# Optimization experiments

Measured on AMD Instinct MI355X. Metric: run time of the kernel, lower is better.

Reference implementation:

```python
import jax, jax.numpy as jnp
import numpy as np

TOTAL_WORDS = 10000
EMBED_LEN = 100
SEQ_LEN = 200
BATCH = 128
UNITS = 256


def setup_inputs() -> dict:
    key = jax.random.key(0)
    ks = jax.random.split(key, 8)
    inputs = jax.random.randint(ks[0], (BATCH, SEQ_LEN), 0, TOTAL_WORDS, dtype=jnp.int32)
    emb = jax.random.normal(ks[1], (TOTAL_WORDS, EMBED_LEN), dtype=jnp.float32) * 0.05
    kernel = jax.random.normal(ks[2], (EMBED_LEN, 3 * UNITS), dtype=jnp.float32) * 0.05
    rkernel = jax.random.normal(ks[3], (UNITS, 3 * UNITS), dtype=jnp.float32) * 0.05
    bias_i = jnp.zeros((3 * UNITS,), dtype=jnp.float32)
    bias_r = jnp.zeros((3 * UNITS,), dtype=jnp.float32)
    w_out = jax.random.normal(ks[4], (UNITS, 1), dtype=jnp.float32) * 0.05
    b_out = jnp.zeros((1,), dtype=jnp.float32)
    return {"inputs": inputs, "emb": emb, "kernel": kernel, "rkernel": rkernel,
            "bias_i": bias_i, "bias_r": bias_r, "w_out": w_out, "b_out": b_out}


def _gru_step(x_t, h, kernel, rkernel, bias_i, bias_r):
    # Keras GRUCell with reset_after=True (TF2 default)
    mx = x_t @ kernel + bias_i          # [B, 3U]
    mh = h @ rkernel + bias_r           # [B, 3U]
    xz, xr, xh = jnp.split(mx, 3, axis=-1)
    hz, hr, hh = jnp.split(mh, 3, axis=-1)
    z = jax.nn.sigmoid(xz + hz)
    r = jax.nn.sigmoid(xr + hr)
    cand = jnp.tanh(xh + r * hh)
    return z * h + (1.0 - z) * cand


def reference(inputs, emb, kernel, rkernel, bias_i, bias_r, w_out, b_out):
    x = emb[inputs]                     # [B, T, E]
    xt = jnp.transpose(x, (1, 0, 2))    # [T, B, E]
    h0 = jnp.zeros((inputs.shape[0], UNITS), dtype=emb.dtype)
    h1 = jnp.zeros((inputs.shape[0], UNITS), dtype=emb.dtype)

    def step(carry, x_t):
        h0, h1 = carry
        # NB: source uses rnn_cell0 for BOTH recurrences, and feeds `word` to both
        h0 = _gru_step(x_t, h0, kernel, rkernel, bias_i, bias_r)
        h1 = _gru_step(x_t, h1, kernel, rkernel, bias_i, bias_r)
        return (h0, h1), None

    (h0, h1), _ = jax.lax.scan(step, (h0, h1), xt)
    logits = h1 @ w_out + b_out         # [B, 1]
    return jax.nn.sigmoid(logits)
```

## Files before the change

kernel.cpp:

```cpp
#include <hip/hip_runtime.h>
#include <stdint.h>

typedef __attribute__((ext_vector_type(8))) short short8;
typedef __attribute__((ext_vector_type(4))) short short4v;
typedef __attribute__((ext_vector_type(4))) float f32x4;
typedef __attribute__((ext_vector_type(4))) int   i32x4;
typedef __attribute__((ext_vector_type(4))) unsigned int u32x4;

#define T_STEPS 200
#define BATCH   128
#define UNITS   256
#define N3      768
#define EMB_D   100

#define NG 128
#define GWAVES 16

#define W8_BYTES  (48 * 4 * 64 * 16)
#define WFX_ELEMS (48 * 4 * 64 * 8)

#define NLOG2E  -1.4426950408889634f
#define N2LOG2E -2.8853900817779268f

#if __has_builtin(__builtin_amdgcn_exp2f)
#define EXP2(x) __builtin_amdgcn_exp2f(x)
#else
#define EXP2(x) __expf((x) * 0.6931471805599453f)
#endif

__device__ __forceinline__ unsigned short f2bf(float f) {
  unsigned int u = __float_as_uint(f);
  u = (u + 0x7fffu + ((u >> 16) & 1u)) >> 16;
  return (unsigned short)u;
}
__device__ __forceinline__ float sigmoidf_(float x) {
  return __builtin_amdgcn_rcpf(1.0f + __expf(-x));
}

__global__ void prep_kernel(const float* __restrict__ kern,
                            const float* __restrict__ rkern,
                            const float* __restrict__ bias_i,
                            const float* __restrict__ bias_r,
                            signed char* __restrict__ w8,
                            unsigned short* __restrict__ wfx,
                            float* __restrict__ bsum,
                            float* __restrict__ cm) {
  int b = blockIdx.x;
  int tid = threadIdx.x;
  if (b < 48) {
    __shared__ float red[256];
    __shared__ float cmv[16];
    int ntg = b;
    int col = tid & 15;
    int n = ntg * 16 + col;
    int k0 = (tid >> 4) * 16;
    float m = 0.0f;
#pragma unroll 4
    for (int k = k0; k < k0 + 16; ++k) m = fmaxf(m, fabsf(rkern[k * N3 + n]));
    red[tid] = m;
    __syncthreads();
    if (tid < 16) {
      float mm = red[tid];
#pragma unroll
      for (int s = 1; s < 16; ++s) mm = fmaxf(mm, red[tid + 16 * s]);
      mm = (mm > 0.0f) ? mm : 1.0f;
      cmv[tid] = mm;
      cm[n] = mm;
    }
    __syncthreads();
    int l = tid & 63, kc = tid >> 6;
    int nn = ntg * 16 + (l & 15);
    float inv127 = 127.0f / cmv[l & 15];
    union { signed char c[16]; i32x4 v; } pk;
#pragma unroll
    for (int e = 0; e < 16; ++e) {
      int k = kc * 64 + (e & 3) + ((l >> 4) & 3) * 4 + ((e >> 2) & 3) * 16;
      float v = rintf(rkern[k * N3 + nn] * inv127);
      v = fminf(127.0f, fmaxf(-127.0f, v));
      pk.c[e] = (signed char)(int)v;
    }
    *(i32x4*)&w8[ntg * 4096 + tid * 16] = pk.v;
  } else {
    int i = (b - 48) * 256 + tid;
    if (i < WFX_ELEMS) {
      int e = i & 7, l = (i >> 3) & 63, ks = (i >> 9) & 3, nt = i >> 11;
      int k = ks * 32 + (e >> 2) * 16 + ((l >> 4) & 3) * 4 + (e & 3);
      int n = nt * 16 + (l & 15);
      float gf = (n < 2 * UNITS) ? NLOG2E : N2LOG2E;
      wfx[i] = (k < EMB_D) ? f2bf(kern[k * N3 + n] * gf) : (unsigned short)0;
    } else if (i < WFX_ELEMS + N3) {
      int c = i - WFX_ELEMS;
      float gf = (c < 2 * UNITS) ? NLOG2E : N2LOG2E;
      bsum[c] = (bias_i[c] + ((c < 2 * UNITS) ? bias_r[c] : 0.0f)) * gf;
    }
  }
}

__global__ __launch_bounds__(256) void mx_kernel(
    const int* __restrict__ inputs, const float* __restrict__ emb,
    const unsigned short* __restrict__ wfx, const float* __restrict__ bsum,
    unsigned int* __restrict__ MXzr, unsigned short* __restrict__ MXc) {
  __shared__ unsigned short Af[4 * 64 * 8];
  __shared__ unsigned short stg[3 * 16 * 256];
  int tile = blockIdx.x;
  int tid = threadIdx.x;
  int lane = tid & 63;
  int wv = tid >> 6;
  {
    short8 z = {0, 0, 0, 0, 0, 0, 0, 0};
    ((short8*)Af)[tid] = z;
  }
  __syncthreads();
  for (int i = tid; i < 512; i += 256) {
    int r = i >> 5, c4 = i & 31;
    if (c4 < 25) {
      int m = tile * 16 + r;
      int ti = m >> 7, b = m & 127;
      int word = inputs[b * T_STEPS + ti];
      f32x4 v = *(const f32x4*)(emb + word * EMB_D + c4 * 4);
      int c = c4 * 4;
      int idx0 = ((c >> 5) * 64 + (r + 16 * ((c >> 2) & 3))) * 8 + ((c >> 4) & 1) * 4;
      short4v p = {(short)f2bf(v.x), (short)f2bf(v.y), (short)f2bf(v.z), (short)f2bf(v.w)};
      *(short4v*)&Af[idx0] = p;
    }
  }
  __syncthreads();
  short8 a0 = ((short8*)Af)[0 * 64 + lane];
  short8 a1 = ((short8*)Af)[1 * 64 + lane];
  short8 a2 = ((short8*)Af)[2 * 64 + lane];
  short8 a3 = ((short8*)Af)[3 * 64 + lane];
  int r0 = (lane >> 4) * 4;
  for (int q = 0; q < 12; ++q) {
    int nt = wv * 12 + q;
    f32x4 acc = {0.f, 0.f, 0.f, 0.f};
    const short8* bp = (const short8*)(wfx) + (nt * 4) * 64 + lane;
    acc = __builtin_amdgcn_mfma_f32_16x16x32_bf16(a0, bp[0],   acc, 0, 0, 0);
    acc = __builtin_amdgcn_mfma_f32_16x16x32_bf16(a1, bp[64],  acc, 0, 0, 0);
    acc = __builtin_amdgcn_mfma_f32_16x16x32_bf16(a2, bp[128], acc, 0, 0, 0);
    acc = __builtin_amdgcn_mfma_f32_16x16x32_bf16(a3, bp[192], acc, 0, 0, 0);
    int col = nt * 16 + (lane & 15);
    float bs = bsum[col];
    int gate = col >> 8, u = col & 255;
    int base = gate * 4096 + r0 * 256 + u;
#pragma unroll
    for (int j = 0; j < 4; ++j) stg[base + j * 256] = f2bf(acc[j] + bs);
  }
  __syncthreads();
  for (int i = tid; i < 4096; i += 256) {
    int r = i >> 8, u = i & 255;
    size_t m = (size_t)tile * 16 + r;
    unsigned int z = stg[r * 256 + u];
    unsigned int rr = stg[4096 + r * 256 + u];
    unsigned int c = stg[8192 + r * 256 + u];
    MXzr[m * 256 + u] = z | (rr << 16);
    MXc[m * 256 + u] = (unsigned short)c;
  }
}

__global__ __launch_bounds__(1024) void gru_kernel(
    const unsigned int* __restrict__ MXzr, const unsigned short* __restrict__ MXc,
    const signed char* __restrict__ w8,
    const float* __restrict__ cm, const float* __restrict__ bias_r,
    const float* __restrict__ w_out, const float* __restrict__ b_out,
    float* __restrict__ out) {
  __shared__ i32x4 hAv[2][4 * 64];
  __shared__ float hout[UNITS];

  int g = blockIdx.x;
  int tid = threadIdx.x;
  int lane = tid & 63;
  int wv = tid >> 6;

  i32x4 bz[4], br[4], bc[4];
  {
    const i32x4* wsrc = (const i32x4*)w8 + lane;
#pragma unroll
    for (int kc = 0; kc < 4; ++kc) {
      bz[kc] = wsrc[(size_t)((wv)*4 + kc) * 64];
      br[kc] = wsrc[(size_t)((16 + wv) * 4 + kc) * 64];
      bc[kc] = wsrc[(size_t)((32 + wv) * 4 + kc) * 64];
    }
  }
  if (tid < 512) { i32x4 z = {0, 0, 0, 0}; ((i32x4*)hAv)[tid] = z; }

  int l15 = lane & 15;
  int u = wv * 16 + l15;
  const float inv = 1.0f / (127.0f * 127.0f);
  float szp = cm[u] * inv * NLOG2E;
  float srp = cm[u + UNITS] * inv * NLOG2E;
  float scp = cm[u + 2 * UNITS] * inv * N2LOG2E;
  float brcp = bias_r[2 * UNITS + u] * N2LOG2E;

  int hwb = (u >> 6) * 1024 + (16 * ((u >> 2) & 3)) * 16 + (u & 3) + 4 * ((u >> 4) & 3);

  float h = 0.0f;
  const unsigned int* mzr = MXzr + (size_t)g * 256 + u;
  const unsigned short* mc = MXc + (size_t)g * 256 + u;
  const size_t mxstride = (size_t)BATCH * 256;
  const float MAGIC = 12582912.0f;

  unsigned int vzr = *mzr;  mzr += mxstride;
  unsigned int vc  = *mc;   mc  += mxstride;

  __syncthreads();

  for (int t = 0; t < T_STEPS; ++t) {
    unsigned int nzr = *mzr;  mzr += mxstride;
    unsigned int nc  = *mc;   mc  += mxstride;

    const i32x4* hp = &hAv[t & 1][0];
    i32x4 af0 = hp[0 * 64 + lane];
    i32x4 af1 = hp[1 * 64 + lane];
    i32x4 af2 = hp[2 * 64 + lane];
    i32x4 af3 = hp[3 * 64 + lane];

    i32x4 az = {0, 0, 0, 0}, ar = {0, 0, 0, 0}, ac = {0, 0, 0, 0};
    az = __builtin_amdgcn_mfma_i32_16x16x64_i8(af0, bz[0], az, 0, 0, 0);
    ar = __builtin_amdgcn_mfma_i32_16x16x64_i8(af0, br[0], ar, 0, 0, 0);
    ac = __builtin_amdgcn_mfma_i32_16x16x64_i8(af0, bc[0], ac, 0, 0, 0);
    az = __builtin_amdgcn_mfma_i32_16x16x64_i8(af1, bz[1], az, 0, 0, 0);
    ar = __builtin_amdgcn_mfma_i32_16x16x64_i8(af1, br[1], ar, 0, 0, 0);
    ac = __builtin_amdgcn_mfma_i32_16x16x64_i8(af1, bc[1], ac, 0, 0, 0);
    az = __builtin_amdgcn_mfma_i32_16x16x64_i8(af2, bz[2], az, 0, 0, 0);
    ar = __builtin_amdgcn_mfma_i32_16x16x64_i8(af2, br[2], ar, 0, 0, 0);
    ac = __builtin_amdgcn_mfma_i32_16x16x64_i8(af2, bc[2], ac, 0, 0, 0);
    az = __builtin_amdgcn_mfma_i32_16x16x64_i8(af3, bz[3], az, 0, 0, 0);
    ar = __builtin_amdgcn_mfma_i32_16x16x64_i8(af3, br[3], ar, 0, 0, 0);
    ac = __builtin_amdgcn_mfma_i32_16x16x64_i8(af3, bc[3], ac, 0, 0, 0);

    float zi = (float)az[0];
    float ri = (float)ar[0];
    float ci = (float)ac[0];
    float xz = __uint_as_float(vzr << 16);
    float xr = __uint_as_float(vzr & 0xffff0000u);
    float xc = __uint_as_float(((unsigned int)vc) << 16);
    float tz = 1.0f + EXP2(fminf(__fmaf_rn(zi, szp, xz), 30.0f));
    float tr = 1.0f + EXP2(fminf(__fmaf_rn(ri, srp, xr), 30.0f));
    float R  = __builtin_amdgcn_rcpf(tz * tr);
    float zg = tr * R;
    float rg = tz * R;
    float mcv = __fmaf_rn(ci, scp, brcp);
    float tc = 1.0f + EXP2(fminf(__fmaf_rn(rg, mcv, xc), 60.0f));
    float cand = __fmaf_rn(2.0f, __builtin_amdgcn_rcpf(tc), -1.0f);
    h = __fmaf_rn(zg, h - cand, cand);
    if (lane < 16) {
      float q = __fmaf_rn(h, 127.0f, MAGIC);
      ((signed char*)hAv)[(((t & 1) ^ 1) * 4096) + hwb] = (signed char)(__float_as_uint(q) & 0xFF);
    }
    vzr = nzr;
    vc  = nc;
    __syncthreads();
  }

  if (lane < 16) hout[u] = h;
  __syncthreads();
  if (tid < 64) {
    float p = 0.0f;
#pragma unroll
    for (int k = 0; k < 4; ++k) p += hout[tid + 64 * k] * w_out[tid + 64 * k];
    p += __shfl_down(p, 32, 64);
    p += __shfl_down(p, 16, 64);
    p += __shfl_down(p, 8, 64);
    p += __shfl_down(p, 4, 64);
    p += __shfl_down(p, 2, 64);
    p += __shfl_down(p, 1, 64);
    if (tid == 0) out[g] = sigmoidf_(p + b_out[0]);
  }
}

extern "C" void kernel_launch(void* const* d_in, const int* in_sizes, int n_in,
                              void* d_out, int out_size, void* d_ws, size_t ws_size,
                              hipStream_t stream) {
  const int*   inputs = (const int*)d_in[0];
  const float* emb    = (const float*)d_in[1];
  const float* kern   = (const float*)d_in[2];
  const float* rkern  = (const float*)d_in[3];
  const float* bias_i = (const float*)d_in[4];
  const float* bias_r = (const float*)d_in[5];
  const float* w_out  = (const float*)d_in[6];
  const float* b_out  = (const float*)d_in[7];
  float* out = (float*)d_out;

  char* ws = (char*)d_ws;
  size_t off = 0;
  size_t mxn = (size_t)T_STEPS * BATCH * 256;
  unsigned int*   MXzr = (unsigned int*)(ws + off);   off += mxn * 4;
  unsigned short* MXc  = (unsigned short*)(ws + off); off += mxn * 2;
  signed char*    w8   = (signed char*)(ws + off);    off += (size_t)W8_BYTES;
  unsigned short* wfx  = (unsigned short*)(ws + off); off += (size_t)WFX_ELEMS * 2;
  float* cm   = (float*)(ws + off); off += (size_t)N3 * 4;
  float* bsum = (float*)(ws + off); off += (size_t)N3 * 4;
  if (off > ws_size) return;

  int prep_blocks = 48 + (WFX_ELEMS + N3 + 255) / 256;
  prep_kernel<<<dim3(prep_blocks), dim3(256), 0, stream>>>(
      kern, rkern, bias_i, bias_r, w8, wfx, bsum, cm);
  mx_kernel<<<dim3(1600), dim3(256), 0, stream>>>(inputs, emb, wfx, bsum, MXzr, MXc);
  gru_kernel<<<dim3(NG), dim3(1024), 0, stream>>>(MXzr, MXc, w8, cm, bias_r, w_out, b_out, out);
}
```

Measured before the change: 151.7 us.

## Halve GRU block waves with two unit tiles per wave; write MX directly

The recurrent GRU kernel now uses 8 waves of 512 threads, each wave handling two 16-unit tiles. It issues 24 int8 MFMAs per step and uses ds_bpermute to spread the column results so 32 lanes each own one unit, aiming to make the per-step block barrier cheaper. The input-projection kernel drops its LDS staging buffer: it computes z/r/c tiles together and writes packed bf16 outputs straight to global memory. The clamp on the candidate exponent is also removed, which relies on exp2 overflow to infinity still giving the correct tanh limit.

New measurement: 159.8 us. 1.05x slower.

```diff
diff --git a/kernel.cpp b/kernel.cpp
--- a/kernel.cpp
+++ b/kernel.cpp
@@ -5,7 +5,6 @@
 typedef __attribute__((ext_vector_type(4))) short short4v;
 typedef __attribute__((ext_vector_type(4))) float f32x4;
 typedef __attribute__((ext_vector_type(4))) int   i32x4;
-typedef __attribute__((ext_vector_type(4))) unsigned int u32x4;
 
 #define T_STEPS 200
 #define BATCH   128
@@ -14,7 +13,7 @@
 #define EMB_D   100
 
 #define NG 128
-#define GWAVES 16
+#define GWAVES 8
 
 #define W8_BYTES  (48 * 4 * 64 * 16)
 #define WFX_ELEMS (48 * 4 * 64 * 8)
@@ -101,7 +100,6 @@
     const unsigned short* __restrict__ wfx, const float* __restrict__ bsum,
     unsigned int* __restrict__ MXzr, unsigned short* __restrict__ MXc) {
   __shared__ unsigned short Af[4 * 64 * 8];
-  __shared__ unsigned short stg[3 * 16 * 256];
   int tile = blockIdx.x;
   int tid = threadIdx.x;
   int lane = tid & 63;
@@ -130,34 +128,40 @@
   short8 a2 = ((short8*)Af)[2 * 64 + lane];
   short8 a3 = ((short8*)Af)[3 * 64 + lane];
   int r0 = (lane >> 4) * 4;
-  for (int q = 0; q < 12; ++q) {
-    int nt = wv * 12 + q;
-    f32x4 acc = {0.f, 0.f, 0.f, 0.f};
-    const short8* bp = (const short8*)(wfx) + (nt * 4) * 64 + lane;
-    acc = __builtin_amdgcn_mfma_f32_16x16x32_bf16(a0, bp[0],   acc, 0, 0, 0);
-    acc = __builtin_amdgcn_mfma_f32_16x16x32_bf16(a1, bp[64],  acc, 0, 0, 0);
-    acc = __builtin_amdgcn_mfma_f32_16x16x32_bf16(a2, bp[128], acc, 0, 0, 0);
-    acc = __builtin_amdgcn_mfma_f32_16x16x32_bf16(a3, bp[192], acc, 0, 0, 0);
-    int col = nt * 16 + (lane & 15);
-    float bs = bsum[col];
-    int gate = col >> 8, u = col & 255;
-    int base = gate * 4096 + r0 * 256 + u;
-#pragma unroll
-    for (int j = 0; j < 4; ++j) stg[base + j * 256] = f2bf(acc[j] + bs);
-  }
-  __syncthreads();
-  for (int i = tid; i < 4096; i += 256) {
-    int r = i >> 8, u = i & 255;
-    size_t m = (size_t)tile * 16 + r;
-    unsigned int z = stg[r * 256 + u];
-    unsigned int rr = stg[4096 + r * 256 + u];
-    unsigned int c = stg[8192 + r * 256 + u];
-    MXzr[m * 256 + u] = z | (rr << 16);
-    MXc[m * 256 + u] = (unsigned short)c;
-  }
-}
-
-__global__ __launch_bounds__(1024) void gru_kernel(
+#pragma unroll
+  for (int p = 0; p < 4; ++p) {
+    int trp = wv * 4 + p;
+    int u = trp * 16 + (lane & 15);
+    float bsz = bsum[u];
+    float bsr = bsum[u + UNITS];
+    float bsc = bsum[u + 2 * UNITS];
+    f32x4 az = {0.f, 0.f, 0.f, 0.f}, ar = {0.f, 0.f, 0.f, 0.f}, ac = {0.f, 0.f, 0.f, 0.f};
+    const short8* bpz = (const short8*)(wfx) + (trp * 4) * 64 + lane;
+    const short8* bpr = (const short8*)(wfx) + ((16 + trp) * 4) * 64 + lane;
+    const short8* bpc = (const short8*)(wfx) + ((32 + trp) * 4) * 64 + lane;
+    az = __builtin_amdgcn_mfma_f32_16x16x32_bf16(a0, bpz[0],   az, 0, 0, 0);
+    ar = __builtin_amdgcn_mfma_f32_16x16x32_bf16(a0, bpr[0],   ar, 0, 0, 0);
+    ac = __builtin_amdgcn_mfma_f32_16x16x32_bf16(a0, bpc[0],   ac, 0, 0, 0);
+    az = __builtin_amdgcn_mfma_f32_16x16x32_bf16(a1, bpz[64],  az, 0, 0, 0);
+    ar = __builtin_amdgcn_mfma_f32_16x16x32_bf16(a1, bpr[64],  ar, 0, 0, 0);
+    ac = __builtin_amdgcn_mfma_f32_16x16x32_bf16(a1, bpc[64],  ac, 0, 0, 0);
+    az = __builtin_amdgcn_mfma_f32_16x16x32_bf16(a2, bpz[128], az, 0, 0, 0);
+    ar = __builtin_amdgcn_mfma_f32_16x16x32_bf16(a2, bpr[128], ar, 0, 0, 0);
+    ac = __builtin_amdgcn_mfma_f32_16x16x32_bf16(a2, bpc[128], ac, 0, 0, 0);
+    az = __builtin_amdgcn_mfma_f32_16x16x32_bf16(a3, bpz[192], az, 0, 0, 0);
+    ar = __builtin_amdgcn_mfma_f32_16x16x32_bf16(a3, bpr[192], ar, 0, 0, 0);
+    ac = __builtin_amdgcn_mfma_f32_16x16x32_bf16(a3, bpc[192], ac, 0, 0, 0);
+#pragma unroll
+    for (int j = 0; j < 4; ++j) {
+      size_t m = (size_t)tile * 16 + r0 + j;
+      unsigned int zr = (unsigned int)f2bf(az[j] + bsz) | ((unsigned int)f2bf(ar[j] + bsr) << 16);
+      MXzr[m * 256 + u] = zr;
+      MXc[m * 256 + u] = f2bf(ac[j] + bsc);
+    }
+  }
+}
+
+__global__ __launch_bounds__(512, 2) void gru_kernel(
     const unsigned int* __restrict__ MXzr, const unsigned short* __restrict__ MXc,
     const signed char* __restrict__ w8,
     const float* __restrict__ cm, const float* __restrict__ bias_r,
@@ -169,22 +173,24 @@
   int g = blockIdx.x;
   int tid = threadIdx.x;
   int lane = tid & 63;
-  int wv = tid >> 6;
-
-  i32x4 bz[4], br[4], bc[4];
+  int w = tid >> 6;
+
+  i32x4 bz0[4], bz1[4], br0[4], br1[4], bc0[4], bc1[4];
   {
     const i32x4* wsrc = (const i32x4*)w8 + lane;
 #pragma unroll
     for (int kc = 0; kc < 4; ++kc) {
-      bz[kc] = wsrc[(size_t)((wv)*4 + kc) * 64];
-      br[kc] = wsrc[(size_t)((16 + wv) * 4 + kc) * 64];
-      bc[kc] = wsrc[(size_t)((32 + wv) * 4 + kc) * 64];
-    }
-  }
-  if (tid < 512) { i32x4 z = {0, 0, 0, 0}; ((i32x4*)hAv)[tid] = z; }
-
-  int l15 = lane & 15;
-  int u = wv * 16 + l15;
+      bz0[kc] = wsrc[(size_t)((2 * w) * 4 + kc) * 64];
+      bz1[kc] = wsrc[(size_t)((2 * w + 1) * 4 + kc) * 64];
+      br0[kc] = wsrc[(size_t)((16 + 2 * w) * 4 + kc) * 64];
+      br1[kc] = wsrc[(size_t)((17 + 2 * w) * 4 + kc) * 64];
+      bc0[kc] = wsrc[(size_t)((32 + 2 * w) * 4 + kc) * 64];
+      bc1[kc] = wsrc[(size_t)((33 + 2 * w) * 4 + kc) * 64];
+    }
+  }
+  { i32x4 z = {0, 0, 0, 0}; ((i32x4*)hAv)[tid] = z; }
+
+  int u = w * 32 + (lane & 31);
   const float inv = 1.0f / (127.0f * 127.0f);
   float szp = cm[u] * inv * NLOG2E;
   float srp = cm[u + UNITS] * inv * NLOG2E;
@@ -193,6 +199,9 @@
 
   int hwb = (u >> 6) * 1024 + (16 * ((u >> 2) & 3)) * 16 + (u & 3) + 4 * ((u >> 4) & 3);
 
+  int bpi = (lane & 15) * 4;
+  int qhi = (lane >> 4) & 1;
+
   float h = 0.0f;
   const unsigned int* mzr = MXzr + (size_t)g * 256 + u;
   const unsigned short* mc = MXc + (size_t)g * 256 + u;
@@ -214,23 +223,44 @@
     i32x4 af2 = hp[2 * 64 + lane];
     i32x4 af3 = hp[3 * 64 + lane];
 
-    i32x4 az = {0, 0, 0, 0}, ar = {0, 0, 0, 0}, ac = {0, 0, 0, 0};
-    az = __builtin_amdgcn_mfma_i32_16x16x64_i8(af0, bz[0], az, 0, 0, 0);
-    ar = __builtin_amdgcn_mfma_i32_16x16x64_i8(af0, br[0], ar, 0, 0, 0);
-    ac = __builtin_amdgcn_mfma_i32_16x16x64_i8(af0, bc[0], ac, 0, 0, 0);
-    az = __builtin_amdgcn_mfma_i32_16x16x64_i8(af1, bz[1], az, 0, 0, 0);
-    ar = __builtin_amdgcn_mfma_i32_16x16x64_i8(af1, br[1], ar, 0, 0, 0);
-    ac = __builtin_amdgcn_mfma_i32_16x16x64_i8(af1, bc[1], ac, 0, 0, 0);
-    az = __builtin_amdgcn_mfma_i32_16x16x64_i8(af2, bz[2], az, 0, 0, 0);
-    ar = __builtin_amdgcn_mfma_i32_16x16x64_i8(af2, br[2], ar, 0, 0, 0);
-    ac = __builtin_amdgcn_mfma_i32_16x16x64_i8(af2, bc[2], ac, 0, 0, 0);
-    az = __builtin_amdgcn_mfma_i32_16x16x64_i8(af3, bz[3], az, 0, 0, 0);
-    ar = __builtin_amdgcn_mfma_i32_16x16x64_i8(af3, br[3], ar, 0, 0, 0);
-    ac = __builtin_amdgcn_mfma_i32_16x16x64_i8(af3, bc[3], ac, 0, 0, 0);
-
-    float zi = (float)az[0];
-    float ri = (float)ar[0];
-    float ci = (float)ac[0];
+    i32x4 az0 = {0, 0, 0, 0}, az1 = {0, 0, 0, 0};
+    i32x4 ar0 = {0, 0, 0, 0}, ar1 = {0, 0, 0, 0};
+    i32x4 ac0 = {0, 0, 0, 0}, ac1 = {0, 0, 0, 0};
+    az0 = __builtin_amdgcn_mfma_i32_16x16x64_i8(af0, bz0[0], az0, 0, 0, 0);
+    az1 = __builtin_amdgcn_mfma_i32_16x16x64_i8(af0, bz1[0], az1, 0, 0, 0);
+    ar0 = __builtin_amdgcn_mfma_i32_16x16x64_i8(af0, br0[0], ar0, 0, 0, 0);
+    ar1 = __builtin_amdgcn_mfma_i32_16x16x64_i8(af0, br1[0], ar1, 0, 0, 0);
+    ac0 = __builtin_amdgcn_mfma_i32_16x16x64_i8(af0, bc0[0], ac0, 0, 0, 0);
+    ac1 = __builtin_amdgcn_mfma_i32_16x16x64_i8(af0, bc1[0], ac1, 0, 0, 0);
+    az0 = __builtin_amdgcn_mfma_i32_16x16x64_i8(af1, bz0[1], az0, 0, 0, 0);
+    az1 = __builtin_amdgcn_mfma_i32_16x16x64_i8(af1, bz1[1], az1, 0, 0, 0);
+    ar0 = __builtin_amdgcn_mfma_i32_16x16x64_i8(af1, br0[1], ar0, 0, 0, 0);
+    ar1 = __builtin_amdgcn_mfma_i32_16x16x64_i8(af1, br1[1], ar1, 0, 0, 0);
+    ac0 = __builtin_amdgcn_mfma_i32_16x16x64_i8(af1, bc0[1], ac0, 0, 0, 0);
+    ac1 = __builtin_amdgcn_mfma_i32_16x16x64_i8(af1, bc1[1], ac1, 0, 0, 0);
+    az0 = __builtin_amdgcn_mfma_i32_16x16x64_i8(af2, bz0[2], az0, 0, 0, 0);
+    az1 = __builtin_amdgcn_mfma_i32_16x16x64_i8(af2, bz1[2], az1, 0, 0, 0);
+    ar0 = __builtin_amdgcn_mfma_i32_16x16x64_i8(af2, br0[2], ar0, 0, 0, 0);
+    ar1 = __builtin_amdgcn_mfma_i32_16x16x64_i8(af2, br1[2], ar1, 0, 0, 0);
+    ac0 = __builtin_amdgcn_mfma_i32_16x16x64_i8(af2, bc0[2], ac0, 0, 0, 0);
+    ac1 = __builtin_amdgcn_mfma_i32_16x16x64_i8(af2, bc1[2], ac1, 0, 0, 0);
+    az0 = __builtin_amdgcn_mfma_i32_16x16x64_i8(af3, bz0[3], az0, 0, 0, 0);
+    az1 = __builtin_amdgcn_mfma_i32_16x16x64_i8(af3, bz1[3], az1, 0, 0, 0);
+    ar0 = __builtin_amdgcn_mfma_i32_16x16x64_i8(af3, br0[3], ar0, 0, 0, 0);
+    ar1 = __builtin_amdgcn_mfma_i32_16x16x64_i8(af3, br1[3], ar1, 0, 0, 0);
+    ac0 = __builtin_amdgcn_mfma_i32_16x16x64_i8(af3, bc0[3], ac0, 0, 0, 0);
+    ac1 = __builtin_amdgcn_mfma_i32_16x16x64_i8(af3, bc1[3], ac1, 0, 0, 0);
+
+    int zi0 = __builtin_amdgcn_ds_bpermute(bpi, az0[0]);
+    int zi1 = __builtin_amdgcn_ds_bpermute(bpi, az1[0]);
+    int ri0 = __builtin_amdgcn_ds_bpermute(bpi, ar0[0]);
+    int ri1 = __builtin_amdgcn_ds_bpermute(bpi, ar1[0]);
+    int ci0 = __builtin_amdgcn_ds_bpermute(bpi, ac0[0]);
+    int ci1 = __builtin_amdgcn_ds_bpermute(bpi, ac1[0]);
+    float zi = (float)(qhi ? zi1 : zi0);
+    float ri = (float)(qhi ? ri1 : ri0);
+    float ci = (float)(qhi ? ci1 : ci0);
+
     float xz = __uint_as_float(vzr << 16);
     float xr = __uint_as_float(vzr & 0xffff0000u);
     float xc = __uint_as_float(((unsigned int)vc) << 16);
@@ -240,10 +270,10 @@
     float zg = tr * R;
     float rg = tz * R;
     float mcv = __fmaf_rn(ci, scp, brcp);
-    float tc = 1.0f + EXP2(fminf(__fmaf_rn(rg, mcv, xc), 60.0f));
+    float tc = 1.0f + EXP2(__fmaf_rn(rg, mcv, xc));
     float cand = __fmaf_rn(2.0f, __builtin_amdgcn_rcpf(tc), -1.0f);
     h = __fmaf_rn(zg, h - cand, cand);
-    if (lane < 16) {
+    if (lane < 32) {
       float q = __fmaf_rn(h, 127.0f, MAGIC);
       ((signed char*)hAv)[(((t & 1) ^ 1) * 4096) + hwb] = (signed char)(__float_as_uint(q) & 0xFF);
     }
@@ -252,7 +282,7 @@
     __syncthreads();
   }
 
-  if (lane < 16) hout[u] = h;
+  if (lane < 32) hout[u] = h;
   __syncthreads();
   if (tid < 64) {
     float p = 0.0f;
@@ -296,5 +326,5 @@
   prep_kernel<<<dim3(prep_blocks), dim3(256), 0, stream>>>(
       kern, rkern, bias_i, bias_r, w8, wfx, bsum, cm);
   mx_kernel<<<dim3(1600), dim3(256), 0, stream>>>(inputs, emb, wfx, bsum, MXzr, MXc);
-  gru_kernel<<<dim3(NG), dim3(1024), 0, stream>>>(MXzr, MXc, w8, cm, bias_r, w_out, b_out, out);
-}
+  gru_kernel<<<dim3(NG), dim3(512), 0, stream>>>(MXzr, MXc, w8, cm, bias_r, w_out, b_out, out);
+}
```

## Concentrate GRU gate math in four waves via LDS exchange, fuse mx stores

Applied to the files above, without the earlier changes.

The recurrent kernel now writes each wave's MFMA outputs to a shared LDS buffer, adds a second barrier per step, and has only waves 0,5,10,15 do the gate nonlinearities, each across all 64 lanes instead of 16 lanes per wave. Only those waves prefetch the per-step input projections. The aim is to cut redundant per-wave VALU work and global loads, at the cost of one extra barrier per timestep and a serialized gate phase. The input-projection kernel also computes z/r/c tiles together and stores straight to global, dropping the LDS staging buffer and its barrier. The tanh exponent clamp is removed.

New measurement: 169.2 us. 1.11x slower.

```diff
diff --git a/kernel.cpp b/kernel.cpp
--- a/kernel.cpp
+++ b/kernel.cpp
@@ -5,7 +5,6 @@
 typedef __attribute__((ext_vector_type(4))) short short4v;
 typedef __attribute__((ext_vector_type(4))) float f32x4;
 typedef __attribute__((ext_vector_type(4))) int   i32x4;
-typedef __attribute__((ext_vector_type(4))) unsigned int u32x4;
 
 #define T_STEPS 200
 #define BATCH   128
@@ -101,7 +100,6 @@
     const unsigned short* __restrict__ wfx, const float* __restrict__ bsum,
     unsigned int* __restrict__ MXzr, unsigned short* __restrict__ MXc) {
   __shared__ unsigned short Af[4 * 64 * 8];
-  __shared__ unsigned short stg[3 * 16 * 256];
   int tile = blockIdx.x;
   int tid = threadIdx.x;
   int lane = tid & 63;
@@ -130,30 +128,36 @@
   short8 a2 = ((short8*)Af)[2 * 64 + lane];
   short8 a3 = ((short8*)Af)[3 * 64 + lane];
   int r0 = (lane >> 4) * 4;
-  for (int q = 0; q < 12; ++q) {
-    int nt = wv * 12 + q;
-    f32x4 acc = {0.f, 0.f, 0.f, 0.f};
-    const short8* bp = (const short8*)(wfx) + (nt * 4) * 64 + lane;
-    acc = __builtin_amdgcn_mfma_f32_16x16x32_bf16(a0, bp[0],   acc, 0, 0, 0);
-    acc = __builtin_amdgcn_mfma_f32_16x16x32_bf16(a1, bp[64],  acc, 0, 0, 0);
-    acc = __builtin_amdgcn_mfma_f32_16x16x32_bf16(a2, bp[128], acc, 0, 0, 0);
-    acc = __builtin_amdgcn_mfma_f32_16x16x32_bf16(a3, bp[192], acc, 0, 0, 0);
-    int col = nt * 16 + (lane & 15);
-    float bs = bsum[col];
-    int gate = col >> 8, u = col & 255;
-    int base = gate * 4096 + r0 * 256 + u;
-#pragma unroll
-    for (int j = 0; j < 4; ++j) stg[base + j * 256] = f2bf(acc[j] + bs);
-  }
-  __syncthreads();
-  for (int i = tid; i < 4096; i += 256) {
-    int r = i >> 8, u = i & 255;
-    size_t m = (size_t)tile * 16 + r;
-    unsigned int z = stg[r * 256 + u];
-    unsigned int rr = stg[4096 + r * 256 + u];
-    unsigned int c = stg[8192 + r * 256 + u];
-    MXzr[m * 256 + u] = z | (rr << 16);
-    MXc[m * 256 + u] = (unsigned short)c;
+#pragma unroll
+  for (int p = 0; p < 4; ++p) {
+    int trp = wv * 4 + p;
+    int u = trp * 16 + (lane & 15);
+    float bsz = bsum[u];
+    float bsr = bsum[u + UNITS];
+    float bsc = bsum[u + 2 * UNITS];
+    f32x4 az = {0.f, 0.f, 0.f, 0.f}, ar = {0.f, 0.f, 0.f, 0.f}, ac = {0.f, 0.f, 0.f, 0.f};
+    const short8* bpz = (const short8*)(wfx) + (trp * 4) * 64 + lane;
+    const short8* bpr = (const short8*)(wfx) + ((16 + trp) * 4) * 64 + lane;
+    const short8* bpc = (const short8*)(wfx) + ((32 + trp) * 4) * 64 + lane;
+    az = __builtin_amdgcn_mfma_f32_16x16x32_bf16(a0, bpz[0],   az, 0, 0, 0);
+    ar = __builtin_amdgcn_mfma_f32_16x16x32_bf16(a0, bpr[0],   ar, 0, 0, 0);
+    ac = __builtin_amdgcn_mfma_f32_16x16x32_bf16(a0, bpc[0],   ac, 0, 0, 0);
+    az = __builtin_amdgcn_mfma_f32_16x16x32_bf16(a1, bpz[64],  az, 0, 0, 0);
+    ar = __builtin_amdgcn_mfma_f32_16x16x32_bf16(a1, bpr[64],  ar, 0, 0, 0);
+    ac = __builtin_amdgcn_mfma_f32_16x16x32_bf16(a1, bpc[64],  ac, 0, 0, 0);
+    az = __builtin_amdgcn_mfma_f32_16x16x32_bf16(a2, bpz[128], az, 0, 0, 0);
+    ar = __builtin_amdgcn_mfma_f32_16x16x32_bf16(a2, bpr[128], ar, 0, 0, 0);
+    ac = __builtin_amdgcn_mfma_f32_16x16x32_bf16(a2, bpc[128], ac, 0, 0, 0);
+    az = __builtin_amdgcn_mfma_f32_16x16x32_bf16(a3, bpz[192], az, 0, 0, 0);
+    ar = __builtin_amdgcn_mfma_f32_16x16x32_bf16(a3, bpr[192], ar, 0, 0, 0);
+    ac = __builtin_amdgcn_mfma_f32_16x16x32_bf16(a3, bpc[192], ac, 0, 0, 0);
+#pragma unroll
+    for (int j = 0; j < 4; ++j) {
+      size_t m = (size_t)tile * 16 + r0 + j;
+      unsigned int zr = (unsigned int)f2bf(az[j] + bsz) | ((unsigned int)f2bf(ar[j] + bsr) << 16);
+      MXzr[m * 256 + u] = zr;
+      MXc[m * 256 + u] = f2bf(ac[j] + bsc);
+    }
   }
 }
 
@@ -164,33 +168,40 @@
     const float* __restrict__ w_out, const float* __restrict__ b_out,
     float* __restrict__ out) {
   __shared__ i32x4 hAv[2][4 * 64];
+  __shared__ int zrc[GWAVES * 48];
   __shared__ float hout[UNITS];
 
   int g = blockIdx.x;
   int tid = threadIdx.x;
   int lane = tid & 63;
-  int wv = tid >> 6;
+  int w = tid >> 6;
 
   i32x4 bz[4], br[4], bc[4];
   {
     const i32x4* wsrc = (const i32x4*)w8 + lane;
 #pragma unroll
     for (int kc = 0; kc < 4; ++kc) {
-      bz[kc] = wsrc[(size_t)((wv)*4 + kc) * 64];
-      br[kc] = wsrc[(size_t)((16 + wv) * 4 + kc) * 64];
-      bc[kc] = wsrc[(size_t)((32 + wv) * 4 + kc) * 64];
+      bz[kc] = wsrc[(size_t)((w)*4 + kc) * 64];
+      br[kc] = wsrc[(size_t)((16 + w) * 4 + kc) * 64];
+      bc[kc] = wsrc[(size_t)((32 + w) * 4 + kc) * 64];
     }
   }
   if (tid < 512) { i32x4 z = {0, 0, 0, 0}; ((i32x4*)hAv)[tid] = z; }
 
-  int l15 = lane & 15;
-  int u = wv * 16 + l15;
-  const float inv = 1.0f / (127.0f * 127.0f);
-  float szp = cm[u] * inv * NLOG2E;
-  float srp = cm[u + UNITS] * inv * NLOG2E;
-  float scp = cm[u + 2 * UNITS] * inv * N2LOG2E;
-  float brcp = bias_r[2 * UNITS + u] * N2LOG2E;
-
+  bool is_gate = (w % 5) == 0;
+  int gw = w / 5;
+  int u = gw * 64 + lane;
+
+  float szp = 0.f, srp = 0.f, scp = 0.f, brcp = 0.f;
+  if (is_gate) {
+    const float inv = 1.0f / (127.0f * 127.0f);
+    szp = cm[u] * inv * NLOG2E;
+    srp = cm[u + UNITS] * inv * NLOG2E;
+    scp = cm[u + 2 * UNITS] * inv * N2LOG2E;
+    brcp = bias_r[2 * UNITS + u] * N2LOG2E;
+  }
+
+  int zaddr = (u >> 4) * 48 + (u & 15);
   int hwb = (u >> 6) * 1024 + (16 * ((u >> 2) & 3)) * 16 + (u & 3) + 4 * ((u >> 4) & 3);
 
   float h = 0.0f;
@@ -199,14 +210,16 @@
   const size_t mxstride = (size_t)BATCH * 256;
   const float MAGIC = 12582912.0f;
 
-  unsigned int vzr = *mzr;  mzr += mxstride;
-  unsigned int vc  = *mc;   mc  += mxstride;
+  unsigned int vzr = 0, vc = 0;
+  if (is_gate) { vzr = *mzr; vc = *mc; }
+  mzr += mxstride; mc += mxstride;
 
   __syncthreads();
 
   for (int t = 0; t < T_STEPS; ++t) {
-    unsigned int nzr = *mzr;  mzr += mxstride;
-    unsigned int nc  = *mc;   mc  += mxstride;
+    unsigned int nzr = 0, nc = 0;
+    if (is_gate) { nzr = *mzr; nc = *mc; }
+    mzr += mxstride; mc += mxstride;
 
     const i32x4* hp = &hAv[t & 1][0];
     i32x4 af0 = hp[0 * 64 + lane];
@@ -228,22 +241,29 @@
     ar = __builtin_amdgcn_mfma_i32_16x16x64_i8(af3, br[3], ar, 0, 0, 0);
     ac = __builtin_amdgcn_mfma_i32_16x16x64_i8(af3, bc[3], ac, 0, 0, 0);
 
-    float zi = (float)az[0];
-    float ri = (float)ar[0];
-    float ci = (float)ac[0];
-    float xz = __uint_as_float(vzr << 16);
-    float xr = __uint_as_float(vzr & 0xffff0000u);
-    float xc = __uint_as_float(((unsigned int)vc) << 16);
-    float tz = 1.0f + EXP2(fminf(__fmaf_rn(zi, szp, xz), 30.0f));
-    float tr = 1.0f + EXP2(fminf(__fmaf_rn(ri, srp, xr), 30.0f));
-    float R  = __builtin_amdgcn_rcpf(tz * tr);
-    float zg = tr * R;
-    float rg = tz * R;
-    float mcv = __fmaf_rn(ci, scp, brcp);
-    float tc = 1.0f + EXP2(fminf(__fmaf_rn(rg, mcv, xc), 60.0f));
-    float cand = __fmaf_rn(2.0f, __builtin_amdgcn_rcpf(tc), -1.0f);
-    h = __fmaf_rn(zg, h - cand, cand);
     if (lane < 16) {
+      zrc[w * 48 + lane]      = az[0];
+      zrc[w * 48 + 16 + lane] = ar[0];
+      zrc[w * 48 + 32 + lane] = ac[0];
+    }
+    __syncthreads();
+
+    if (is_gate) {
+      float zi = (float)zrc[zaddr];
+      float ri = (float)zrc[zaddr + 16];
+      float ci = (float)zrc[zaddr + 32];
+      float xz = __uint_as_float(vzr << 16);
+      float xr = __uint_as_float(vzr & 0xffff0000u);
+      float xc = __uint_as_float(((unsigned int)vc) << 16);
+      float tz = 1.0f + EXP2(fminf(__fmaf_rn(zi, szp, xz), 30.0f));
+      float tr = 1.0f + EXP2(fminf(__fmaf_rn(ri, srp, xr), 30.0f));
+      float R  = __builtin_amdgcn_rcpf(tz * tr);
+      float zg = tr * R;
+      float rg = tz * R;
+      float mcv = __fmaf_rn(ci, scp, brcp);
+      float tc = 1.0f + EXP2(__fmaf_rn(rg, mcv, xc));
+      float cand = __fmaf_rn(2.0f, __builtin_amdgcn_rcpf(tc), -1.0f);
+      h = __fmaf_rn(zg, h - cand, cand);
       float q = __fmaf_rn(h, 127.0f, MAGIC);
       ((signed char*)hAv)[(((t & 1) ^ 1) * 4096) + hwb] = (signed char)(__float_as_uint(q) & 0xFF);
     }
@@ -252,7 +272,7 @@
     __syncthreads();
   }
 
-  if (lane < 16) hout[u] = h;
+  if (is_gate) hout[u] = h;
   __syncthreads();
   if (tid < 64) {
     float p = 0.0f;
```
